# Performance work log

Measured on AMD Instinct MI355X. Metric: run time of the kernel, lower is better.

## Reference

```python
import math
import jax, jax.numpy as jnp
import numpy as np

B, S, DM, H = 4, 1024, 1024, 16
D = DM // H


def setup_inputs() -> dict:
    key = jax.random.key(0)
    ks = jax.random.split(key, 8)
    q = jax.random.normal(ks[0], (B, S, DM), dtype=jnp.float32)
    k = jax.random.normal(ks[1], (B, S, DM), dtype=jnp.float32)
    v = jax.random.normal(ks[2], (B, S, DM), dtype=jnp.float32)
    w_scale = 0.02
    Wq = jax.random.normal(ks[3], (DM, DM), dtype=jnp.float32) * w_scale
    Wk = jax.random.normal(ks[4], (DM, DM), dtype=jnp.float32) * w_scale
    Wv = jax.random.normal(ks[5], (DM, DM), dtype=jnp.float32) * w_scale
    Wo = jax.random.normal(ks[6], (DM, DM), dtype=jnp.float32) * w_scale
    bq = jnp.zeros((DM,), jnp.float32)
    bk = jnp.zeros((DM,), jnp.float32)
    bv = jnp.zeros((DM,), jnp.float32)
    bo = jnp.zeros((DM,), jnp.float32)
    # mask==1 means masked (upper triangle above the diagonal)
    causal_mask = jnp.triu(jnp.ones((S, S), jnp.int32), k=1)
    return {"q": q, "k": k, "v": v, "Wq": Wq, "bq": bq, "Wk": Wk, "bk": bk,
            "Wv": Wv, "bv": bv, "Wo": Wo, "bo": bo, "causal_mask": causal_mask}


def reference(q, k, v, Wq, bq, Wk, bk, Wv, bv, Wo, bo, causal_mask):
    Bn, Sq, Dm = q.shape
    # projections (torch Linear: x @ W.T + b)
    qh = (q @ Wq.T + bq).reshape(Bn, Sq, H, D).transpose(0, 2, 1, 3)  # [B,H,S,D]
    kh = (k @ Wk.T + bk).reshape(Bn, -1, H, D).transpose(0, 2, 1, 3)
    vh = (v @ Wv.T + bv).reshape(Bn, -1, H, D).transpose(0, 2, 1, 3)
    # NOTE: module divides by sqrt(d_model), not sqrt(d_head)
    score = jnp.einsum('bhqd,bhkd->bhqk', qh, kh) / math.sqrt(Dm)
    score = jnp.where(causal_mask == 1, jnp.float32(-1e9), score)
    attn_weights = jax.nn.softmax(score, axis=-1)  # dropout is identity in eval
    x = jnp.einsum('bhqk,bhkd->bhqd', attn_weights, vh)
    x = x.transpose(0, 2, 1, 3).reshape(Bn, Sq, Dm)
    x = x @ Wo.T + bo
    present = jnp.stack([kh, vh])  # [2,B,H,S,D]
    return (x, present, attn_weights)
```

## Files before the change

kernel.cpp:

```cpp
#include <hip/hip_runtime.h>


typedef __bf16 bf16x8 __attribute__((ext_vector_type(8)));
typedef float f32x4 __attribute__((ext_vector_type(4)));
typedef unsigned short u16;
typedef unsigned int u32;

#define B_ 4
#define S_ 1024
#define DM_ 1024
#define H_ 16
#define D_ 64

static constexpr size_t N_QKV = (size_t)B_ * S_ * DM_;
static constexpr size_t N_W   = (size_t)DM_ * DM_;

static constexpr size_t QB_OFF = 0;
static constexpr size_t KB_OFF = QB_OFF + N_QKV;
static constexpr size_t VB_OFF = KB_OFF + N_QKV;
static constexpr size_t WQ_OFF = VB_OFF + N_QKV;
static constexpr size_t WK_OFF = WQ_OFF + N_W;
static constexpr size_t WV_OFF = WK_OFF + N_W;
static constexpr size_t WO_OFF = WV_OFF + N_W;
static constexpr size_t QH_OFF = WO_OFF + N_W;
static constexpr size_t KH_OFF = QH_OFF + N_QKV;
static constexpr size_t VT_OFF = KH_OFF + N_QKV;
static constexpr size_t XH_OFF = VT_OFF + N_QKV;

static constexpr size_t P0_OFF = N_QKV;
static constexpr size_t P1_OFF = 2 * N_QKV;
static constexpr size_t AW_OFF = 3 * N_QKV;

__device__ __forceinline__ u16 f2bf(float f) {
    u32 u = __float_as_uint(f);
    u += 0x7FFFu + ((u >> 16) & 1u);
    return (u16)(u >> 16);
}

__device__ __forceinline__ f32x4 zero4() {
    f32x4 z = {0.f, 0.f, 0.f, 0.f};
    return z;
}

__device__ __forceinline__ void async16(const void* g, void* lds) {
    __builtin_amdgcn_global_load_lds(
        (__attribute__((address_space(1))) u32*)g,
        (__attribute__((address_space(3))) u32*)lds,
        16, 0, 0);
}

__device__ __forceinline__ int swzf(int f) {
    return f ^ (((f >> 7) & 7) << 4);
}
__device__ __forceinline__ int swz16(int row, int elem) {
    return row * 64 + (elem ^ ((row & 7) << 3));
}

__global__ __launch_bounds__(256) void cvt_kernel(
    const float* __restrict__ q, const float* __restrict__ k, const float* __restrict__ v,
    const float* __restrict__ wq, const float* __restrict__ wk, const float* __restrict__ wv,
    const float* __restrict__ wo, u16* __restrict__ ws)
{
    const int seg = blockIdx.y;
    const float* src; u16* dst; size_t n;
    switch (seg) {
        case 0: src = q;  dst = ws + QB_OFF; n = N_QKV; break;
        case 1: src = k;  dst = ws + KB_OFF; n = N_QKV; break;
        case 2: src = v;  dst = ws + VB_OFF; n = N_QKV; break;
        case 3: src = wq; dst = ws + WQ_OFF; n = N_W;   break;
        case 4: src = wk; dst = ws + WK_OFF; n = N_W;   break;
        case 5: src = wv; dst = ws + WV_OFF; n = N_W;   break;
        default: src = wo; dst = ws + WO_OFF; n = N_W;  break;
    }
    const size_t idx = ((size_t)blockIdx.x * 256 + threadIdx.x) * 4;
    if (idx >= n) return;
    float4 f = *(const float4*)(src + idx);
    u32 p0 = (u32)f2bf(f.x) | ((u32)f2bf(f.y) << 16);
    u32 p1 = (u32)f2bf(f.z) | ((u32)f2bf(f.w) << 16);
    *(uint2*)(dst + idx) = make_uint2(p0, p1);
}

__device__ __forceinline__ void gemm_mainloop(
    const u16* __restrict__ A, const u16* __restrict__ W, int K,
    int row0, int col0, u16* As, u16* Bs, f32x4 (&acc)[4][4])
{
    const int tid = threadIdx.x;
    const int lane = tid & 63;
    const int w = tid >> 6;
    const int wm = w & 1, wn = w >> 1;
    const int l15 = lane & 15;
    const int acol = (lane >> 4) * 8;

    for (int k0 = 0; k0 < K; k0 += 32) {
#pragma unroll
        for (int j = 0; j < 2; ++j) {
            const int f = (j * 256 + tid) * 16;
            const int r = f >> 6, cb = f & 63;
            async16((const char*)A + ((size_t)(row0 + r) * K + k0) * 2 + cb,
                    (char*)As + j * 4096 + w * 1024);
            async16((const char*)W + ((size_t)(col0 + r) * K + k0) * 2 + cb,
                    (char*)Bs + j * 4096 + w * 1024);
        }
        __syncthreads();
        bf16x8 af[4], bfr[4];
#pragma unroll
        for (int t = 0; t < 4; ++t) {
            af[t]  = *(const bf16x8*)(As + (wm * 64 + t * 16 + l15) * 32 + acol);
            bfr[t] = *(const bf16x8*)(Bs + (wn * 64 + t * 16 + l15) * 32 + acol);
        }
#pragma unroll
        for (int tm = 0; tm < 4; ++tm)
#pragma unroll
            for (int tn = 0; tn < 4; ++tn)
                acc[tm][tn] = __builtin_amdgcn_mfma_f32_16x16x32_bf16(
                    af[tm], bfr[tn], acc[tm][tn], 0, 0, 0);
        __syncthreads();
    }
}

__global__ __launch_bounds__(256) void proj_kernel(
    u16* __restrict__ ws, const float* __restrict__ bq, const float* __restrict__ bk,
    const float* __restrict__ bv, float* __restrict__ out)
{
    const int mode = blockIdx.z;
    const u16* A = ws + QB_OFF + (size_t)mode * N_QKV;
    const u16* W = ws + WQ_OFF + (size_t)mode * N_W;
    const float* bias = (mode == 0) ? bq : (mode == 1 ? bk : bv);
    __shared__ __align__(16) u16 As[128 * 32];
    __shared__ __align__(16) u16 Bs[128 * 32];
    f32x4 acc[4][4];
#pragma unroll
    for (int i = 0; i < 4; ++i)
#pragma unroll
        for (int j = 0; j < 4; ++j) acc[i][j] = zero4();

    const int row0 = blockIdx.x * 128, col0 = blockIdx.y * 128;
    gemm_mainloop(A, W, DM_, row0, col0, As, Bs, acc);

    const int lane = threadIdx.x & 63, w = threadIdx.x >> 6;
    const int wm = w & 1, wn = w >> 1;
    const int quad = lane >> 4, l15 = lane & 15;
#pragma unroll
    for (int tm = 0; tm < 4; ++tm)
#pragma unroll
        for (int tn = 0; tn < 4; ++tn)
#pragma unroll
            for (int i = 0; i < 4; ++i) {
                const int m = row0 + wm * 64 + tm * 16 + quad * 4 + i;
                const int n = col0 + wn * 64 + tn * 16 + l15;
                const float val = acc[tm][tn][i] + bias[n];
                const int b = m >> 10, s = m & (S_ - 1);
                const int h = n >> 6, d = n & 63;
                const size_t hidx = (((size_t)b * H_ + h) * S_ + s) * D_ + d;
                if (mode == 0) {
                    ws[QH_OFF + hidx] = f2bf(val);
                } else if (mode == 1) {
                    out[P0_OFF + hidx] = val;
                    ws[KH_OFF + hidx] = f2bf(val);
                } else {
                    out[P1_OFF + hidx] = val;
                    ws[VT_OFF + (((size_t)b * H_ + h) * D_ + d) * S_ + s] = f2bf(val);
                }
            }
}

__global__ __launch_bounds__(256) void attn_kernel(u16* __restrict__ ws, float* __restrict__ out)
{
    const int qt = blockIdx.x;
    const int h  = blockIdx.y;
    const int b  = blockIdx.z;
    const int bh = b * H_ + h;
    const int q0 = qt * 64;

    const u16* Qg  = ws + QH_OFF + ((size_t)bh * S_ + q0) * D_;
    const u16* Kg  = ws + KH_OFF + (size_t)bh * S_ * D_;
    const u16* Vtg = ws + VT_OFF + (size_t)bh * D_ * S_;
    float* AW = out + AW_OFF + ((size_t)bh * S_ + q0) * S_;
    u16* XH = ws + XH_OFF;

    __shared__ __align__(16) u16 Qs[64 * 64];
    __shared__ __align__(16) u16 Ks[64 * 64];
    __shared__ __align__(16) u16 Vs[64 * 64];
    __shared__ __align__(16) u16 Ps[4][16 * 64];

    const int tid = threadIdx.x;
    const int lane = tid & 63;
    const int w = tid >> 6;
    const int quad = lane >> 4, l15 = lane & 15;

#pragma unroll
    for (int j = 0; j < 2; ++j) {
        const int f = (j * 256 + tid) * 16;
        async16((const char*)Qg + swzf(f), (char*)Qs + j * 4096 + w * 1024);
    }
    __syncthreads();

    bf16x8 aq[2];
#pragma unroll
    for (int kk = 0; kk < 2; ++kk)
        aq[kk] = *(const bf16x8*)(Qs + swz16(w * 16 + l15, kk * 32 + quad * 8));

    const int ntiles = qt + 1;
    const float scale = 0.03125f;
    const int qrow = q0 + w * 16 + quad * 4;

    float ps[4] = {0.f, 0.f, 0.f, 0.f};
    for (int t = 0; t < ntiles; ++t) {
        __syncthreads();
#pragma unroll
        for (int j = 0; j < 2; ++j) {
            const int f = (j * 256 + tid) * 16;
            async16((const char*)Kg + (size_t)t * 8192 + swzf(f),
                    (char*)Ks + j * 4096 + w * 1024);
        }
        __syncthreads();
        f32x4 sa[4];
        sa[0] = sa[1] = sa[2] = sa[3] = zero4();
#pragma unroll
        for (int kk = 0; kk < 2; ++kk) {
#pragma unroll
            for (int n = 0; n < 4; ++n) {
                bf16x8 bk = *(const bf16x8*)(Ks + swz16(n * 16 + l15, kk * 32 + quad * 8));
                sa[n] = __builtin_amdgcn_mfma_f32_16x16x32_bf16(aq[kk], bk, sa[n], 0, 0, 0);
            }
        }
#pragma unroll
        for (int n = 0; n < 4; ++n) {
            const int kcol = t * 64 + n * 16 + l15;
#pragma unroll
            for (int i = 0; i < 4; ++i) {
                float e = (kcol <= qrow + i) ? __expf(sa[n][i] * scale) : 0.f;
                ps[i] += e;
            }
        }
    }

    float rinv[4];
#pragma unroll
    for (int i = 0; i < 4; ++i) {
        float s = ps[i];
        s += __shfl_xor(s, 1);
        s += __shfl_xor(s, 2);
        s += __shfl_xor(s, 4);
        s += __shfl_xor(s, 8);
        rinv[i] = 1.f / s;
    }

    f32x4 oacc[4];
    oacc[0] = oacc[1] = oacc[2] = oacc[3] = zero4();

    for (int t = 0; t < ntiles; ++t) {
        __syncthreads();
#pragma unroll
        for (int j = 0; j < 2; ++j) {
            const int f = (j * 256 + tid) * 16;
            async16((const char*)Kg + (size_t)t * 8192 + swzf(f),
                    (char*)Ks + j * 4096 + w * 1024);
            const int d = f >> 7;
            const int cb = (f & 127) ^ ((d & 7) << 4);
            async16((const char*)Vtg + (size_t)d * (S_ * 2) + (size_t)t * 128 + cb,
                    (char*)Vs + j * 4096 + w * 1024);
        }
        __syncthreads();
        f32x4 sa[4];
        sa[0] = sa[1] = sa[2] = sa[3] = zero4();
#pragma unroll
        for (int kk = 0; kk < 2; ++kk) {
#pragma unroll
            for (int n = 0; n < 4; ++n) {
                bf16x8 bk = *(const bf16x8*)(Ks + swz16(n * 16 + l15, kk * 32 + quad * 8));
                sa[n] = __builtin_amdgcn_mfma_f32_16x16x32_bf16(aq[kk], bk, sa[n], 0, 0, 0);
            }
        }
#pragma unroll
        for (int n = 0; n < 4; ++n) {
            const int kcol = t * 64 + n * 16 + l15;
#pragma unroll
            for (int i = 0; i < 4; ++i) {
                float e = (kcol <= qrow + i) ? __expf(sa[n][i] * scale) : 0.f;
                float wgt = e * rinv[i];
                AW[(size_t)(w * 16 + quad * 4 + i) * S_ + kcol] = wgt;
                Ps[w][swz16(quad * 4 + i, n * 16 + l15)] = f2bf(wgt);
            }
        }
#pragma unroll
        for (int kk = 0; kk < 2; ++kk) {
            bf16x8 ap = *(const bf16x8*)(&Ps[w][swz16(l15, kk * 32 + quad * 8)]);
#pragma unroll
            for (int n = 0; n < 4; ++n) {
                bf16x8 bv = *(const bf16x8*)(Vs + swz16(n * 16 + l15, kk * 32 + quad * 8));
                oacc[n] = __builtin_amdgcn_mfma_f32_16x16x32_bf16(ap, bv, oacc[n], 0, 0, 0);
            }
        }
    }

#pragma unroll
    for (int n = 0; n < 4; ++n)
#pragma unroll
        for (int i = 0; i < 4; ++i) {
            const int qq = q0 + w * 16 + quad * 4 + i;
            const int dc = h * 64 + n * 16 + l15;
            XH[((size_t)b * S_ + qq) * DM_ + dc] = f2bf(oacc[n][i]);
        }

    const int zc0 = ntiles * 64;
    const int Z = S_ - zc0;
    if (Z > 0) {
        const int total = 64 * Z;
        for (int idx = tid * 4; idx < total; idx += 1024) {
            const int r = idx / Z, c = idx - r * Z;
            *(float4*)(&AW[(size_t)r * S_ + zc0 + c]) = make_float4(0.f, 0.f, 0.f, 0.f);
        }
    }
}

__global__ __launch_bounds__(256) void outproj_kernel(
    u16* __restrict__ ws, const float* __restrict__ bo, float* __restrict__ out)
{
    const u16* A = ws + XH_OFF;
    const u16* W = ws + WO_OFF;
    __shared__ __align__(16) u16 As[128 * 32];
    __shared__ __align__(16) u16 Bs[128 * 32];
    f32x4 acc[4][4];
#pragma unroll
    for (int i = 0; i < 4; ++i)
#pragma unroll
        for (int j = 0; j < 4; ++j) acc[i][j] = zero4();

    const int row0 = blockIdx.x * 128, col0 = blockIdx.y * 128;
    gemm_mainloop(A, W, DM_, row0, col0, As, Bs, acc);

    const int lane = threadIdx.x & 63, w = threadIdx.x >> 6;
    const int wm = w & 1, wn = w >> 1;
    const int quad = lane >> 4, l15 = lane & 15;
#pragma unroll
    for (int tm = 0; tm < 4; ++tm)
#pragma unroll
        for (int tn = 0; tn < 4; ++tn)
#pragma unroll
            for (int i = 0; i < 4; ++i) {
                const int m = row0 + wm * 64 + tm * 16 + quad * 4 + i;
                const int n = col0 + wn * 64 + tn * 16 + l15;
                out[(size_t)m * DM_ + n] = acc[tm][tn][i] + bo[n];
            }
}

extern "C" void kernel_launch(void* const* d_in, const int* in_sizes, int n_in,
                              void* d_out, int out_size, void* d_ws, size_t ws_size,
                              hipStream_t stream) {
    const float* q  = (const float*)d_in[0];
    const float* k  = (const float*)d_in[1];
    const float* v  = (const float*)d_in[2];
    const float* Wq = (const float*)d_in[3];
    const float* bq = (const float*)d_in[4];
    const float* Wk = (const float*)d_in[5];
    const float* bk = (const float*)d_in[6];
    const float* Wv = (const float*)d_in[7];
    const float* bv = (const float*)d_in[8];
    const float* Wo = (const float*)d_in[9];
    const float* bo = (const float*)d_in[10];

    u16* ws = (u16*)d_ws;
    float* out = (float*)d_out;
    dim3 blk(256);

    cvt_kernel<<<dim3(4096, 7, 1), blk, 0, stream>>>(q, k, v, Wq, Wk, Wv, Wo, ws);
    proj_kernel<<<dim3(32, 8, 3), blk, 0, stream>>>(ws, bq, bk, bv, out);
    attn_kernel<<<dim3(S_ / 64, H_, B_), blk, 0, stream>>>(ws, out);
    outproj_kernel<<<dim3(32, 8, 1), blk, 0, stream>>>(ws, bo, out);
}
```

Before: 497.8 us.

## Stage V transpose through LDS, reverse attention tile order, add MFMA priority hints

Result: no change. 492.3 us (-1.1%).

```diff
diff --git a/kernel.cpp b/kernel.cpp
--- a/kernel.cpp
+++ b/kernel.cpp
@@ -126,8 +126,10 @@
     const u16* A = ws + QB_OFF + (size_t)mode * N_QKV;
     const u16* W = ws + WQ_OFF + (size_t)mode * N_W;
     const float* bias = (mode == 0) ? bq : (mode == 1 ? bk : bv);
-    __shared__ __align__(16) u16 As[128 * 32];
-    __shared__ __align__(16) u16 Bs[128 * 32];
+    __shared__ __align__(16) u16 smem[128 * 128];
+    u16* As = smem;
+    u16* Bs = smem + 128 * 32;
+    u16* T  = smem;
     f32x4 acc[4][4];
 #pragma unroll
     for (int i = 0; i < 4; ++i)
@@ -137,7 +139,8 @@
     const int row0 = blockIdx.x * 128, col0 = blockIdx.y * 128;
     gemm_mainloop(A, W, DM_, row0, col0, As, Bs, acc);
 
-    const int lane = threadIdx.x & 63, w = threadIdx.x >> 6;
+    const int tid = threadIdx.x;
+    const int lane = tid & 63, w = tid >> 6;
     const int wm = w & 1, wn = w >> 1;
     const int quad = lane >> 4, l15 = lane & 15;
 #pragma unroll
@@ -159,14 +162,31 @@
                     ws[KH_OFF + hidx] = f2bf(val);
                 } else {
                     out[P1_OFF + hidx] = val;
-                    ws[VT_OFF + (((size_t)b * H_ + h) * D_ + d) * S_ + s] = f2bf(val);
+                    const int r = wn * 64 + tn * 16 + l15;
+                    const int c = wm * 64 + tm * 16 + quad * 4 + i;
+                    T[r * 128 + (c ^ ((r & 15) << 3))] = f2bf(val);
                 }
             }
+
+    if (mode == 2) {
+        __syncthreads();
+        const int b = row0 >> 10;
+        const int s0 = row0 & (S_ - 1);
+#pragma unroll
+        for (int p = 0; p < 8; ++p) {
+            const int r = p * 16 + (tid >> 4);
+            const int c0 = (tid & 15) * 8;
+            const int n = col0 + r;
+            const int h = n >> 6, d = n & 63;
+            bf16x8 vv = *(const bf16x8*)(T + r * 128 + (c0 ^ ((r & 15) << 3)));
+            *(bf16x8*)(ws + VT_OFF + (((size_t)b * H_ + h) * D_ + d) * S_ + s0 + c0) = vv;
+        }
+    }
 }
 
 __global__ __launch_bounds__(256) void attn_kernel(u16* __restrict__ ws, float* __restrict__ out)
 {
-    const int qt = blockIdx.x;
+    const int qt = (S_ / 64 - 1) - blockIdx.x;
     const int h  = blockIdx.y;
     const int b  = blockIdx.z;
     const int bh = b * H_ + h;
@@ -216,6 +236,7 @@
         __syncthreads();
         f32x4 sa[4];
         sa[0] = sa[1] = sa[2] = sa[3] = zero4();
+        __builtin_amdgcn_s_setprio(1);
 #pragma unroll
         for (int kk = 0; kk < 2; ++kk) {
 #pragma unroll
@@ -224,6 +245,7 @@
                 sa[n] = __builtin_amdgcn_mfma_f32_16x16x32_bf16(aq[kk], bk, sa[n], 0, 0, 0);
             }
         }
+        __builtin_amdgcn_s_setprio(0);
 #pragma unroll
         for (int n = 0; n < 4; ++n) {
             const int kcol = t * 64 + n * 16 + l15;
@@ -264,6 +286,7 @@
         __syncthreads();
         f32x4 sa[4];
         sa[0] = sa[1] = sa[2] = sa[3] = zero4();
+        __builtin_amdgcn_s_setprio(1);
 #pragma unroll
         for (int kk = 0; kk < 2; ++kk) {
 #pragma unroll
@@ -272,6 +295,7 @@
                 sa[n] = __builtin_amdgcn_mfma_f32_16x16x32_bf16(aq[kk], bk, sa[n], 0, 0, 0);
             }
         }
+        __builtin_amdgcn_s_setprio(0);
 #pragma unroll
         for (int n = 0; n < 4; ++n) {
             const int kcol = t * 64 + n * 16 + l15;
@@ -283,6 +307,7 @@
                 Ps[w][swz16(quad * 4 + i, n * 16 + l15)] = f2bf(wgt);
             }
         }
+        __builtin_amdgcn_s_setprio(1);
 #pragma unroll
         for (int kk = 0; kk < 2; ++kk) {
             bf16x8 ap = *(const bf16x8*)(&Ps[w][swz16(l15, kk * 32 + quad * 8)]);
@@ -292,6 +317,7 @@
                 oacc[n] = __builtin_amdgcn_mfma_f32_16x16x32_bf16(ap, bv, oacc[n], 0, 0, 0);
             }
         }
+        __builtin_amdgcn_s_setprio(0);
     }
 
 #pragma unroll
```
